# Optimization experiments

Hardware: AMD Instinct MI355X
Metric: run time of the kernel (lower is better)

## Reference

```python
import jax, jax.numpy as jnp
import numpy as np

HEADS = 8
EMBED = 64  # out_channels per head
N_OP = 100000
N_MC = 20000
N_EDGE = 300000
EPS = 1e-16  # matches PyG softmax denominator epsilon


def hetero_gat(x_src, x_dst, edge_index, W, att, n_dst):
    """GAT conv: gather -> per-edge score -> segment softmax over dst -> scatter-sum -> head mean.
    x_src: [Ns, F], x_dst: [Nd, F], edge_index: [2, E] (row0=src, row1=dst),
    W: [HEADS*EMBED, F], att: [1, HEADS, 2*EMBED].
    """
    hs = (x_src @ W.T).reshape(-1, HEADS, EMBED)  # [Ns,H,C]
    hd = (x_dst @ W.T).reshape(-1, HEADS, EMBED)  # [Nd,H,C]
    src, dst = edge_index[0], edge_index[1]
    x_j = hs[src]                                  # [E,H,C] (source/neighbor)
    x_i = hd[dst]                                  # [E,H,C] (destination)
    att_i = att[0, :, :EMBED]                      # [H,C] weights for x_i part of concat
    att_j = att[0, :, EMBED:]                      # [H,C] weights for x_j part
    # (cat([x_i,x_j],-1) * att).sum(-1) without materializing the concat
    alpha = jnp.einsum('ehc,hc->eh', x_i, att_i) + jnp.einsum('ehc,hc->eh', x_j, att_j)
    # segment softmax grouped by destination node
    m = jax.ops.segment_max(alpha, dst, num_segments=n_dst)  # [Nd,H]
    e = jnp.exp(alpha - m[dst])
    s = jax.ops.segment_sum(e, dst, num_segments=n_dst)      # [Nd,H]
    alpha = e / (s[dst] + EPS)                                # [E,H]
    msg = x_j * alpha[..., None]                              # [E,H,C]
    out = jax.ops.segment_sum(msg, dst, num_segments=n_dst)   # [Nd,H,C]
    return out.mean(axis=1)                                   # [Nd,C] multi-head mean


def setup_inputs() -> dict:
    key = jax.random.key(0)
    ks = jax.random.split(key, 12)
    op_nodes = jax.random.normal(ks[0], (N_OP, 4), dtype=jnp.float32)
    mc_nodes = jax.random.normal(ks[1], (N_MC, 2), dtype=jnp.float32)
    src = jax.random.randint(ks[2], (N_EDGE,), 0, N_OP)
    dst = jax.random.randint(ks[3], (N_EDGE,), 0, N_MC)
    edge_index_om = jnp.stack([src, dst]).astype(jnp.int64)
    g = 0.1
    params = {
        'W_op': jax.random.normal(ks[4], (EMBED, 4), dtype=jnp.float32) * g,
        'b_op': jnp.zeros((EMBED,), dtype=jnp.float32),
        'W_mc': jax.random.normal(ks[5], (EMBED, 2), dtype=jnp.float32) * g,
        'b_mc': jnp.zeros((EMBED,), dtype=jnp.float32),
        'W_om': jax.random.normal(ks[6], (HEADS * EMBED, EMBED), dtype=jnp.float32) * g,
        'att_om': jax.random.normal(ks[7], (1, HEADS, 2 * EMBED), dtype=jnp.float32) * g,
        'W_mo': jax.random.normal(ks[8], (HEADS * EMBED, EMBED), dtype=jnp.float32) * g,
        'att_mo': jax.random.normal(ks[9], (1, HEADS, 2 * EMBED), dtype=jnp.float32) * g,
    }
    return {'op_nodes': op_nodes, 'mc_nodes': mc_nodes, 'edge_index_om': edge_index_om, **params}


def reference(op_nodes, mc_nodes, edge_index_om, W_op, b_op, W_mc, b_mc,
              W_om, att_om, W_mo, att_mo):
    h_op = jax.nn.elu(op_nodes @ W_op.T + b_op)   # [N_OP, 64]
    h_mc = jax.nn.elu(mc_nodes @ W_mc.T + b_mc)   # [N_MC, 64]
    # op -> mc
    h_mc_new = hetero_gat(h_op, h_mc, edge_index_om, W_om, att_om, N_MC)
    h_mc = jax.nn.elu(h_mc + h_mc_new)
    # mc -> op (reversed edges)
    edge_index_mo = jnp.stack([edge_index_om[1], edge_index_om[0]])
    h_op_new = hetero_gat(h_mc, h_op, edge_index_mo, W_mo, att_mo, N_OP)
    h_op = jax.nn.elu(h_op + h_op_new)
    return (h_op, h_mc)
```

## Files before the change

kernel.cpp:

```cpp
#include <hip/hip_runtime.h>
#include <hip/hip_bf16.h>

using bf16 = __hip_bfloat16;
typedef __attribute__((ext_vector_type(8))) short short8;
typedef __attribute__((ext_vector_type(4))) float f32x4;

__device__ __forceinline__ unsigned short f2bf(float f) {
  bf16 h = __float2bfloat16(f);
  return *reinterpret_cast<unsigned short*>(&h);
}
__device__ __forceinline__ float bf2f(unsigned short u) {
  return __uint_as_float(((unsigned)u) << 16);
}

__device__ __forceinline__ float loadf(const void* p, int i, int is_f32) {
  if (is_f32) return ((const float*)p)[i];
  return __bfloat162float(((const bf16*)p)[i]);
}

__global__ __launch_bounds__(256) void init_kernel(
    const int* __restrict__ ei, const unsigned short* __restrict__ x,
    int* __restrict__ flags, int* __restrict__ cnt1, int n1,
    int* __restrict__ cnt2, int n2) {
  int t = threadIdx.x;
  int g = blockIdx.x * 256 + t;
  int stride = gridDim.x * 256;
  for (int i = g; i < n1; i += stride) cnt1[i] = 0;
  for (int i = g; i < n2; i += stride) cnt2[i] = 0;
  if (blockIdx.x == 0) {
    __shared__ int red[256];
    int o = 0, big = 0;
    for (int i = t; i < 2048; i += 256) {
      o |= ei[2 * i + 1];
      float v = __uint_as_float(((unsigned)x[2 * i]) << 16);
      if (!(fabsf(v) < 1000.f)) big = 1;
    }
    red[t] = o;
    __syncthreads();
    for (int d = 128; d > 0; d >>= 1) {
      if (t < d) red[t] |= red[t + d];
      __syncthreads();
    }
    int o_all = red[0];
    __syncthreads();
    red[t] = big;
    __syncthreads();
    for (int d = 128; d > 0; d >>= 1) {
      if (t < d) red[t] |= red[t + d];
      __syncthreads();
    }
    if (t == 0) {
      flags[0] = red[0];
      flags[1] = (o_all == 0) ? 1 : 0;
    }
  }
}

__device__ __forceinline__ int edge_src(const int* ei, int E, int e, int i64) {
  return i64 ? ei[2 * e] : ei[e];
}
__device__ __forceinline__ int edge_dst(const int* ei, int E, int e, int i64) {
  return i64 ? ei[2 * E + 2 * e] : ei[E + e];
}

template <int FIN>
__device__ __forceinline__ void node_body4(
    const void* x, const void* W, const void* b, int is_f32,
    const float* vj, bf16* h_out, float* ea_out, int n0, int N) {
  int lane = threadIdx.x & 63;
  float wreg[FIN];
#pragma unroll
  for (int f = 0; f < FIN; ++f) wreg[f] = loadf(W, lane * FIN + f, is_f32);
  float bias = loadf(b, lane, is_f32);
  float vjreg[8];
  if (ea_out) {
#pragma unroll
    for (int h = 0; h < 8; ++h) vjreg[h] = vj[h * 64 + lane];
  }
#pragma unroll
  for (int j = 0; j < 4; ++j) {
    int n = n0 + j;
    if (n >= N) break;
    float acc = bias;
#pragma unroll
    for (int f = 0; f < FIN; ++f)
      acc += loadf(x, n * FIN + f, is_f32) * wreg[f];
    float hv = acc > 0.f ? acc : expm1f(acc);
    h_out[(unsigned)(n << 6) + lane] = __float2bfloat16(hv);
    if (ea_out) {
      float p[8];
#pragma unroll
      for (int h = 0; h < 8; ++h) p[h] = hv * vjreg[h];
#pragma unroll
      for (int i = 0; i < 4; ++i) {
        float send = (lane & 4) ? p[i] : p[i + 4];
        float keep = (lane & 4) ? p[i + 4] : p[i];
        p[i] = keep + __shfl_xor(send, 4, 64);
      }
#pragma unroll
      for (int i = 0; i < 2; ++i) {
        float send = (lane & 2) ? p[i] : p[i + 2];
        float keep = (lane & 2) ? p[i + 2] : p[i];
        p[i] = keep + __shfl_xor(send, 2, 64);
      }
      {
        float send = (lane & 1) ? p[0] : p[1];
        float keep = (lane & 1) ? p[1] : p[0];
        p[0] = keep + __shfl_xor(send, 1, 64);
      }
      p[0] += __shfl_xor(p[0], 8, 64);
      p[0] += __shfl_xor(p[0], 16, 64);
      p[0] += __shfl_xor(p[0], 32, 64);
      if (lane < 8) ea_out[(unsigned)(n << 3) + lane] = __expf(p[0]);
    }
  }
}

__global__ __launch_bounds__(256) void front_kernel(
    const void* __restrict__ x_op, const void* __restrict__ W_op,
    const void* __restrict__ b_op, const void* __restrict__ x_mc,
    const void* __restrict__ W_mc, const void* __restrict__ b_mc,
    const void* __restrict__ W1, const void* __restrict__ att1,
    const void* __restrict__ W2, const void* __restrict__ att2,
    const int* __restrict__ ei, const int* __restrict__ flags,
    float* __restrict__ vj1, bf16* __restrict__ Wrt1, float* __restrict__ vj2,
    bf16* __restrict__ Wrt2, bf16* __restrict__ h_op,
    float* __restrict__ ea_op, bf16* __restrict__ h_mc,
    int* __restrict__ cnt_dst, int* __restrict__ cnt_src, int n_op, int n_mc,
    int E, int nbo, int nbm) {
  int bid = blockIdx.x;
  int is_f32 = flags[0];
  if (bid < nbo) {
    int n0 = bid * 16 + (threadIdx.x >> 6) * 4;
    if (n0 < n_op)
      node_body4<4>(x_op, W_op, b_op, is_f32, vj1, h_op, ea_op, n0, n_op);
  } else if (bid < nbo + nbm) {
    int n0 = (bid - nbo) * 16 + (threadIdx.x >> 6) * 4;
    if (n0 < n_mc)
      node_body4<2>(x_mc, W_mc, b_mc, is_f32, nullptr, h_mc, nullptr, n0, n_mc);
  } else if (bid < nbo + nbm + 256) {
    int pb = bid - nbo - nbm;
    int side = pb >= 128;
    const void* W = side ? W2 : W1;
    const void* att = side ? att2 : att1;
    float* vj = side ? vj2 : vj1;
    bf16* Wrt = side ? Wrt2 : Wrt1;
    int tt = (pb & 127) * 256 + threadIdx.x;
    if (tt < 32768) {
      int c = tt >> 9, k = tt & 511;
      int f = k >> 3, h = k & 7;
      Wrt[tt] = __float2bfloat16(loadf(W, ((h << 6) + c) * 64 + f, is_f32));
    }
    if (tt < 512) {
      int hh = tt >> 6, ff = tt & 63;
      float s = 0.f;
      for (int cc = 0; cc < 64; ++cc)
        s += loadf(att, hh * 128 + 64 + cc, is_f32) *
             loadf(W, ((hh << 6) + cc) * 64 + ff, is_f32);
      vj[tt] = s;
    }
  } else {
    int i64 = flags[1];
    int e = (bid - nbo - nbm - 256) * 256 + threadIdx.x;
    if (e < E) {
      atomicAdd(&cnt_dst[edge_dst(ei, E, e, i64)], 1);
      atomicAdd(&cnt_src[edge_src(ei, E, e, i64)], 1);
    }
  }
}

__global__ __launch_bounds__(256) void scan_bsum2(
    const int* __restrict__ cnt1, int n1, int nb1, const int* __restrict__ cnt2,
    int n2, int* __restrict__ bsum1, int* __restrict__ bsum2) {
  __shared__ int red[256];
  int t = threadIdx.x;
  int side = (int)blockIdx.x >= nb1;
  const int* cnt = side ? cnt2 : cnt1;
  int n = side ? n2 : n1;
  int blk = side ? (blockIdx.x - nb1) : blockIdx.x;
  int base = blk * 2048 + t * 8;
  int s = 0;
#pragma unroll
  for (int i = 0; i < 8; ++i)
    if (base + i < n) s += cnt[base + i];
  red[t] = s;
  __syncthreads();
  for (int d = 128; d > 0; d >>= 1) {
    if (t < d) red[t] += red[t + d];
    __syncthreads();
  }
  if (t == 0) (side ? bsum2 : bsum1)[blk] = red[0];
}

__global__ __launch_bounds__(256) void scan_write2(
    const int* __restrict__ cnt1, int n1, int nb1,
    const int* __restrict__ bsum1, int* __restrict__ offs1,
    int* __restrict__ cur1, const int* __restrict__ cnt2, int n2, int nb2,
    const int* __restrict__ bsum2, int* __restrict__ offs2,
    int* __restrict__ cur2) {
  __shared__ int red[256];
  __shared__ int base_s;
  int t = threadIdx.x;
  int side = (int)blockIdx.x >= nb1;
  const int* cnt = side ? cnt2 : cnt1;
  const int* bsum = side ? bsum2 : bsum1;
  int* offs = side ? offs2 : offs1;
  int* cur = side ? cur2 : cur1;
  int n = side ? n2 : n1;
  int nb = side ? nb2 : nb1;
  int blk = side ? (blockIdx.x - nb1) : blockIdx.x;
  if (t == 0) {
    int b = 0;
    for (int i = 0; i < blk; ++i) b += bsum[i];
    base_s = b;
  }
  int base = blk * 2048 + t * 8;
  int c[8];
  int s = 0;
#pragma unroll
  for (int i = 0; i < 8; ++i) {
    c[i] = (base + i < n) ? cnt[base + i] : 0;
    s += c[i];
  }
  red[t] = s;
  __syncthreads();
  for (int d = 1; d < 256; d <<= 1) {
    int v = red[t];
    int add = (t >= d) ? red[t - d] : 0;
    __syncthreads();
    red[t] = v + add;
    __syncthreads();
  }
  int run = base_s + red[t] - s;
#pragma unroll
  for (int i = 0; i < 8; ++i) {
    if (base + i < n) {
      offs[base + i] = run;
      cur[base + i] = run;
      run += c[i];
    }
  }
  if (blk == nb - 1 && t == 255) offs[n] = base_s + red[255];
}

__global__ __launch_bounds__(256) void fill_edges(
    const int* __restrict__ ei, int E, const int* __restrict__ flags,
    int* __restrict__ cur1, int* __restrict__ srcs1, int* __restrict__ cur2,
    int* __restrict__ srcs2) {
  int i64 = flags[1];
  int e = blockIdx.x * blockDim.x + threadIdx.x;
  if (e < E) {
    int s = edge_src(ei, E, e, i64), d = edge_dst(ei, E, e, i64);
    int p = atomicAdd(&cur1[d], 1);
    srcs1[p] = s;
    int q = atomicAdd(&cur2[s], 1);
    srcs2[q] = d;
  }
}

template <bool WRITE_AJ, bool WRITE_BF>
__global__ __launch_bounds__(256) void gat_fused(
    int Nd, const int* __restrict__ offs, const int* __restrict__ srcs,
    const float* __restrict__ ea, const bf16* __restrict__ h_src,
    const bf16* __restrict__ Wrt, const bf16* __restrict__ h_res,
    float* __restrict__ out_f32, bf16* __restrict__ out_bf,
    const float* __restrict__ vj_next, float* __restrict__ ea_next) {
  __shared__ __align__(16) unsigned short Zl[16 * 520];
  __shared__ int srcs_sw[4][65];
  __shared__ __align__(16) float ew_s[4][528];
  float(*ajp)[16][8] = reinterpret_cast<float(*)[16][8]>(&ew_s[0][0]);

  int t = threadIdx.x;
  int wv = t >> 6, lane = t & 63;
  int d0 = blockIdx.x * 16;
  int sj = lane >> 4;
  int fq = lane & 15;

  int dlo = d0 + wv * 4;
  int wo0 = offs[min(dlo + 0, Nd)];
  int wo1 = offs[min(dlo + 1, Nd)];
  int wo2 = offs[min(dlo + 2, Nd)];
  int wo3 = offs[min(dlo + 3, Nd)];
  int wo4 = offs[min(dlo + 4, Nd)];
  int woj = sj == 0 ? wo0 : sj == 1 ? wo1 : sj == 2 ? wo2 : wo3;
  int woj1 = sj == 0 ? wo1 : sj == 1 ? wo2 : sj == 2 ? wo3 : wo4;

  float z[8][4];
#pragma unroll
  for (int h = 0; h < 8; ++h)
#pragma unroll
    for (int f = 0; f < 4; ++f) z[h][f] = 0.f;
  float s8[8];
#pragma unroll
  for (int h = 0; h < 8; ++h) s8[h] = 0.f;

  const unsigned short* hsrc_u = (const unsigned short*)h_src;

  for (int cb = wo0; cb < wo4; cb += 64) {
    int cn = min(64, wo4 - cb);
    for (int i = lane; i < cn + 1; i += 64)
      srcs_sw[wv][i] = (i < cn) ? srcs[cb + i] : 0;
    for (int i = lane; i < (cn + 1) * 8; i += 64) {
      int e = i >> 3;
      int src2 = (e < cn) ? srcs[cb + e] : 0;
      ew_s[wv][i] = (e < cn) ? ea[((unsigned)src2 << 3) + (i & 7)] : 0.f;
    }
    int c0 = max(cb, woj) - cb;
    int e1 = min(cb + cn, woj1) - cb;
    int rl = max(e1 - c0, 0);
    int rmax = max(rl, __shfl_xor(rl, 16, 64));
    rmax = max(rmax, __shfl_xor(rmax, 32, 64));
    for (int r0 = 0; r0 < rmax; r0 += 4) {
      int i2q[4];
      ushort4 uq[4];
#pragma unroll
      for (int q = 0; q < 4; ++q) {
        int r = r0 + q;
        int i2 = (r < rl) ? (c0 + r) : cn;
        i2q[q] = i2;
        int src = srcs_sw[wv][i2];
        uq[q] = *(const ushort4*)(hsrc_u + (((unsigned)src) << 6) + (fq << 2));
      }
#pragma unroll
      for (int q = 0; q < 4; ++q) {
        int i2 = i2q[q];
        float4 lo4 = *(const float4*)&ew_s[wv][i2 * 8];
        float4 hi4 = *(const float4*)&ew_s[wv][i2 * 8 + 4];
        float x0 = bf2f(uq[q].x), x1 = bf2f(uq[q].y);
        float x2 = bf2f(uq[q].z), x3 = bf2f(uq[q].w);
        z[0][0] += lo4.x * x0; z[0][1] += lo4.x * x1; z[0][2] += lo4.x * x2; z[0][3] += lo4.x * x3;
        z[1][0] += lo4.y * x0; z[1][1] += lo4.y * x1; z[1][2] += lo4.y * x2; z[1][3] += lo4.y * x3;
        z[2][0] += lo4.z * x0; z[2][1] += lo4.z * x1; z[2][2] += lo4.z * x2; z[2][3] += lo4.z * x3;
        z[3][0] += lo4.w * x0; z[3][1] += lo4.w * x1; z[3][2] += lo4.w * x2; z[3][3] += lo4.w * x3;
        z[4][0] += hi4.x * x0; z[4][1] += hi4.x * x1; z[4][2] += hi4.x * x2; z[4][3] += hi4.x * x3;
        z[5][0] += hi4.y * x0; z[5][1] += hi4.y * x1; z[5][2] += hi4.y * x2; z[5][3] += hi4.y * x3;
        z[6][0] += hi4.z * x0; z[6][1] += hi4.z * x1; z[6][2] += hi4.z * x2; z[6][3] += hi4.z * x3;
        z[7][0] += hi4.w * x0; z[7][1] += hi4.w * x1; z[7][2] += hi4.w * x2; z[7][3] += hi4.w * x3;
        s8[0] += lo4.x; s8[1] += lo4.y; s8[2] += lo4.z; s8[3] += lo4.w;
        s8[4] += hi4.x; s8[5] += hi4.y; s8[6] += hi4.z; s8[7] += hi4.w;
      }
    }
  }

  float si[8];
#pragma unroll
  for (int h = 0; h < 8; ++h) si[h] = s8[h] > 0.f ? 1.f / s8[h] : 0.f;
  int row = wv * 4 + sj;
#pragma unroll
  for (int fi = 0; fi < 4; ++fi) {
    int4 pk;
    pk.x = ((int)f2bf(z[1][fi] * si[1]) << 16) | f2bf(z[0][fi] * si[0]);
    pk.y = ((int)f2bf(z[3][fi] * si[3]) << 16) | f2bf(z[2][fi] * si[2]);
    pk.z = ((int)f2bf(z[5][fi] * si[5]) << 16) | f2bf(z[4][fi] * si[4]);
    pk.w = ((int)f2bf(z[7][fi] * si[7]) << 16) | f2bf(z[6][fi] * si[6]);
    *(int4*)&Zl[row * 520 + (fq * 4 + fi) * 8] = pk;
  }

  int arow = lane & 15;
  int kg = lane >> 4;
  int col = wv * 16 + arow;
  float res[4];
#pragma unroll
  for (int r = 0; r < 4; ++r) {
    int d = d0 + kg * 4 + r;
    res[r] = (d < Nd)
                 ? __bfloat162float(h_res[(unsigned)(d << 6) + col])
                 : 0.f;
  }
  __syncthreads();

  f32x4 acc = {0.f, 0.f, 0.f, 0.f};
#pragma unroll
  for (int kt = 0; kt < 16; ++kt) {
    int kbase = kt * 32 + kg * 8;
    short8 a = *(const short8*)&Zl[arow * 520 + kbase];
    short8 b = *(const short8*)&Wrt[(unsigned)((wv * 16 + arow) * 512 + kbase)];
    acc = __builtin_amdgcn_mfma_f32_16x16x32_bf16(a, b, acc, 0, 0, 0);
  }

  float o_r[4];
#pragma unroll
  for (int r = 0; r < 4; ++r) {
    int d = d0 + kg * 4 + r;
    float o = 0.f;
    if (d < Nd) {
      float v = res[r] + 0.125f * acc[r];
      o = v > 0.f ? v : expm1f(v);
      out_f32[(unsigned)(d << 6) + col] = o;
      if (WRITE_BF) out_bf[(unsigned)(d << 6) + col] = __float2bfloat16(o);
    }
    o_r[r] = o;
  }

  if (WRITE_AJ) {
#pragma unroll
    for (int r = 0; r < 4; ++r) {
      int dloc = kg * 4 + r;
      float p[8];
#pragma unroll
      for (int h = 0; h < 8; ++h) p[h] = o_r[r] * vj_next[h * 64 + col];
#pragma unroll
      for (int i = 0; i < 4; ++i) {
        float send = (arow & 4) ? p[i] : p[i + 4];
        float keep = (arow & 4) ? p[i + 4] : p[i];
        p[i] = keep + __shfl_xor(send, 4, 64);
      }
#pragma unroll
      for (int i = 0; i < 2; ++i) {
        float send = (arow & 2) ? p[i] : p[i + 2];
        float keep = (arow & 2) ? p[i + 2] : p[i];
        p[i] = keep + __shfl_xor(send, 2, 64);
      }
      {
        float send = (arow & 1) ? p[0] : p[1];
        float keep = (arow & 1) ? p[1] : p[0];
        p[0] = keep + __shfl_xor(send, 1, 64);
      }
      p[0] += __shfl_xor(p[0], 8, 64);
      if (arow < 8) ajp[wv][dloc][arow] = p[0];
    }
    __syncthreads();
    if (t < 128) {
      int dloc = t >> 3, h = t & 7;
      int d = d0 + dloc;
      if (d < Nd) {
        float s = ajp[0][dloc][h] + ajp[1][dloc][h] + ajp[2][dloc][h] +
                  ajp[3][dloc][h];
        ea_next[(unsigned)(d << 3) + h] = __expf(s);
      }
    }
  }
}

extern "C" void kernel_launch(void* const* d_in, const int* in_sizes, int n_in,
                              void* d_out, int out_size, void* d_ws,
                              size_t ws_size, hipStream_t stream) {
  const void* op_nodes = d_in[0];
  const void* mc_nodes = d_in[1];
  const int* ei        = (const int*)d_in[2];
  const void* W_op     = d_in[3];
  const void* b_op     = d_in[4];
  const void* W_mc     = d_in[5];
  const void* b_mc     = d_in[6];
  const void* W_om     = d_in[7];
  const void* att_om   = d_in[8];
  const void* W_mo     = d_in[9];
  const void* att_mo   = d_in[10];

  int n_op = in_sizes[0] / 4;
  int n_mc = in_sizes[1] / 2;
  int E    = in_sizes[2] / 2;

  char* ws = (char*)d_ws;
  size_t off = 0;
  auto alloc = [&](size_t bytes) -> void* {
    void* p = ws + off;
    off = (off + bytes + 255) & ~(size_t)255;
    return p;
  };
  int* flags   = (int*)alloc(16);
  bf16* h_op   = (bf16*)alloc((size_t)n_op * 64 * 2);
  bf16* h_mc   = (bf16*)alloc((size_t)n_mc * 64 * 2);
  bf16* h_mc2  = (bf16*)alloc((size_t)n_mc * 64 * 2);
  float* ea_op = (float*)alloc((size_t)n_op * 8 * 4);
  float* ea_mc = (float*)alloc((size_t)n_mc * 8 * 4);
  float* vj_om = (float*)alloc(512 * 4);
  float* vj_mo = (float*)alloc(512 * 4);
  bf16* Wrt_om = (bf16*)alloc(32768 * 2);
  bf16* Wrt_mo = (bf16*)alloc(32768 * 2);
  int* cnt1  = (int*)alloc((size_t)n_mc * 4);
  int* cnt2  = (int*)alloc((size_t)n_op * 4);
  int* offs1 = (int*)alloc((size_t)(n_mc + 1) * 4);
  int* cur1  = (int*)alloc((size_t)n_mc * 4);
  int* srcs1 = (int*)alloc((size_t)E * 4);
  int* offs2 = (int*)alloc((size_t)(n_op + 1) * 4);
  int* cur2  = (int*)alloc((size_t)n_op * 4);
  int* srcs2 = (int*)alloc((size_t)E * 4);
  int* bsum1 = (int*)alloc(256 * 4);
  int* bsum2 = (int*)alloc(256 * 4);

  float* out_op = (float*)d_out;
  float* out_mc = out_op + (size_t)n_op * 64;

  init_kernel<<<512, 256, 0, stream>>>(ei, (const unsigned short*)op_nodes,
                                       flags, cnt1, n_mc, cnt2, n_op);

  int nbo = (n_op + 15) / 16, nbm = (n_mc + 15) / 16;
  int nbe = (E + 255) / 256;
  front_kernel<<<nbo + nbm + 256 + nbe, 256, 0, stream>>>(
      op_nodes, W_op, b_op, mc_nodes, W_mc, b_mc, W_om, att_om, W_mo, att_mo,
      ei, flags, vj_om, Wrt_om, vj_mo, Wrt_mo, h_op, ea_op, h_mc, cnt1, cnt2,
      n_op, n_mc, E, nbo, nbm);

  int nb1 = (n_mc + 2047) / 2048, nb2 = (n_op + 2047) / 2048;
  scan_bsum2<<<nb1 + nb2, 256, 0, stream>>>(cnt1, n_mc, nb1, cnt2, n_op, bsum1,
                                            bsum2);
  scan_write2<<<nb1 + nb2, 256, 0, stream>>>(cnt1, n_mc, nb1, bsum1, offs1,
                                             cur1, cnt2, n_op, nb2, bsum2,
                                             offs2, cur2);
  fill_edges<<<nbe, 256, 0, stream>>>(ei, E, flags, cur1, srcs1, cur2, srcs2);

  gat_fused<true, true><<<(n_mc + 15) / 16, 256, 0, stream>>>(
      n_mc, offs1, srcs1, ea_op, h_op, Wrt_om, h_mc, out_mc, h_mc2, vj_mo,
      ea_mc);
  gat_fused<false, false><<<(n_op + 15) / 16, 256, 0, stream>>>(
      n_op, offs2, srcs2, ea_mc, h_mc2, Wrt_mo, h_op, out_op, (bf16*)nullptr,
      (const float*)nullptr, (float*)nullptr);
}
```

Measured before the change: 233.5 us.

## Store edge attention weights in bf16 and gather them directly per edge

Per-source exp attention weights (ea) are now stored as bf16 instead of fp32, halving their footprint. The gather loop no longer stages source indices and weights into per-wave shared memory in 64-edge chunks. Each lane now reads its own source indices and 16-byte weight vectors straight from global memory. This removes the shared staging, its redundant cooperative loads, and the shared-memory footprint, at the cost of more scattered global reads of srcs and ea per lane and reduced precision in the softmax weights.

```diff
diff --git a/kernel.cpp b/kernel.cpp
--- a/kernel.cpp
+++ b/kernel.cpp
@@ -66,7 +66,7 @@
 template <int FIN>
 __device__ __forceinline__ void node_body4(
     const void* x, const void* W, const void* b, int is_f32,
-    const float* vj, bf16* h_out, float* ea_out, int n0, int N) {
+    const float* vj, bf16* h_out, unsigned short* ea_out, int n0, int N) {
   int lane = threadIdx.x & 63;
   float wreg[FIN];
 #pragma unroll
@@ -111,7 +111,7 @@
       p[0] += __shfl_xor(p[0], 8, 64);
       p[0] += __shfl_xor(p[0], 16, 64);
       p[0] += __shfl_xor(p[0], 32, 64);
-      if (lane < 8) ea_out[(unsigned)(n << 3) + lane] = __expf(p[0]);
+      if (lane < 8) ea_out[(unsigned)(n << 3) + lane] = f2bf(__expf(p[0]));
     }
   }
 }
@@ -125,7 +125,7 @@
     const int* __restrict__ ei, const int* __restrict__ flags,
     float* __restrict__ vj1, bf16* __restrict__ Wrt1, float* __restrict__ vj2,
     bf16* __restrict__ Wrt2, bf16* __restrict__ h_op,
-    float* __restrict__ ea_op, bf16* __restrict__ h_mc,
+    unsigned short* __restrict__ ea_op, bf16* __restrict__ h_mc,
     int* __restrict__ cnt_dst, int* __restrict__ cnt_src, int n_op, int n_mc,
     int E, int nbo, int nbm) {
   int bid = blockIdx.x;
@@ -261,14 +261,12 @@
 template <bool WRITE_AJ, bool WRITE_BF>
 __global__ __launch_bounds__(256) void gat_fused(
     int Nd, const int* __restrict__ offs, const int* __restrict__ srcs,
-    const float* __restrict__ ea, const bf16* __restrict__ h_src,
+    const unsigned short* __restrict__ ea, const bf16* __restrict__ h_src,
     const bf16* __restrict__ Wrt, const bf16* __restrict__ h_res,
     float* __restrict__ out_f32, bf16* __restrict__ out_bf,
-    const float* __restrict__ vj_next, float* __restrict__ ea_next) {
+    const float* __restrict__ vj_next, unsigned short* __restrict__ ea_next) {
   __shared__ __align__(16) unsigned short Zl[16 * 520];
-  __shared__ int srcs_sw[4][65];
-  __shared__ __align__(16) float ew_s[4][528];
-  float(*ajp)[16][8] = reinterpret_cast<float(*)[16][8]>(&ew_s[0][0]);
+  __shared__ float ajp[4][16][8];
 
   int t = threadIdx.x;
   int wv = t >> 6, lane = t & 63;
@@ -284,6 +282,7 @@
   int wo4 = offs[min(dlo + 4, Nd)];
   int woj = sj == 0 ? wo0 : sj == 1 ? wo1 : sj == 2 ? wo2 : wo3;
   int woj1 = sj == 0 ? wo1 : sj == 1 ? wo2 : sj == 2 ? wo3 : wo4;
+  int nj = woj1 - woj;
 
   float z[8][4];
 #pragma unroll
@@ -296,48 +295,40 @@
 
   const unsigned short* hsrc_u = (const unsigned short*)h_src;
 
-  for (int cb = wo0; cb < wo4; cb += 64) {
-    int cn = min(64, wo4 - cb);
-    for (int i = lane; i < cn + 1; i += 64)
-      srcs_sw[wv][i] = (i < cn) ? srcs[cb + i] : 0;
-    for (int i = lane; i < (cn + 1) * 8; i += 64) {
-      int e = i >> 3;
-      int src2 = (e < cn) ? srcs[cb + e] : 0;
-      ew_s[wv][i] = (e < cn) ? ea[((unsigned)src2 << 3) + (i & 7)] : 0.f;
-    }
-    int c0 = max(cb, woj) - cb;
-    int e1 = min(cb + cn, woj1) - cb;
-    int rl = max(e1 - c0, 0);
-    int rmax = max(rl, __shfl_xor(rl, 16, 64));
-    rmax = max(rmax, __shfl_xor(rmax, 32, 64));
-    for (int r0 = 0; r0 < rmax; r0 += 4) {
-      int i2q[4];
-      ushort4 uq[4];
-#pragma unroll
-      for (int q = 0; q < 4; ++q) {
-        int r = r0 + q;
-        int i2 = (r < rl) ? (c0 + r) : cn;
-        i2q[q] = i2;
-        int src = srcs_sw[wv][i2];
-        uq[q] = *(const ushort4*)(hsrc_u + (((unsigned)src) << 6) + (fq << 2));
-      }
-#pragma unroll
-      for (int q = 0; q < 4; ++q) {
-        int i2 = i2q[q];
-        float4 lo4 = *(const float4*)&ew_s[wv][i2 * 8];
-        float4 hi4 = *(const float4*)&ew_s[wv][i2 * 8 + 4];
-        float x0 = bf2f(uq[q].x), x1 = bf2f(uq[q].y);
-        float x2 = bf2f(uq[q].z), x3 = bf2f(uq[q].w);
-        z[0][0] += lo4.x * x0; z[0][1] += lo4.x * x1; z[0][2] += lo4.x * x2; z[0][3] += lo4.x * x3;
-        z[1][0] += lo4.y * x0; z[1][1] += lo4.y * x1; z[1][2] += lo4.y * x2; z[1][3] += lo4.y * x3;
-        z[2][0] += lo4.z * x0; z[2][1] += lo4.z * x1; z[2][2] += lo4.z * x2; z[2][3] += lo4.z * x3;
-        z[3][0] += lo4.w * x0; z[3][1] += lo4.w * x1; z[3][2] += lo4.w * x2; z[3][3] += lo4.w * x3;
-        z[4][0] += hi4.x * x0; z[4][1] += hi4.x * x1; z[4][2] += hi4.x * x2; z[4][3] += hi4.x * x3;
-        z[5][0] += hi4.y * x0; z[5][1] += hi4.y * x1; z[5][2] += hi4.y * x2; z[5][3] += hi4.y * x3;
-        z[6][0] += hi4.z * x0; z[6][1] += hi4.z * x1; z[6][2] += hi4.z * x2; z[6][3] += hi4.z * x3;
-        z[7][0] += hi4.w * x0; z[7][1] += hi4.w * x1; z[7][2] += hi4.w * x2; z[7][3] += hi4.w * x3;
-        s8[0] += lo4.x; s8[1] += lo4.y; s8[2] += lo4.z; s8[3] += lo4.w;
-        s8[4] += hi4.x; s8[5] += hi4.y; s8[6] += hi4.z; s8[7] += hi4.w;
+  int rmax = max(nj, __shfl_xor(nj, 16, 64));
+  rmax = max(rmax, __shfl_xor(rmax, 32, 64));
+
+  for (int r0 = 0; r0 < rmax; r0 += 4) {
+    unsigned srcq[4];
+#pragma unroll
+    for (int q = 0; q < 4; ++q) {
+      int r = r0 + q;
+      srcq[q] = (r < nj) ? (unsigned)srcs[woj + r] : 0u;
+    }
+    ushort4 uq[4];
+    short8 eq[4];
+#pragma unroll
+    for (int q = 0; q < 4; ++q) {
+      unsigned s = srcq[q];
+      uq[q] = *(const ushort4*)(hsrc_u + (s << 6) + (fq << 2));
+      eq[q] = *(const short8*)(ea + (s << 3));
+    }
+#pragma unroll
+    for (int q = 0; q < 4; ++q) {
+      bool act = (r0 + q) < nj;
+      float w[8];
+#pragma unroll
+      for (int h = 0; h < 8; ++h)
+        w[h] = act ? bf2f((unsigned short)eq[q][h]) : 0.f;
+      float x0 = bf2f(uq[q].x), x1 = bf2f(uq[q].y);
+      float x2 = bf2f(uq[q].z), x3 = bf2f(uq[q].w);
+#pragma unroll
+      for (int h = 0; h < 8; ++h) {
+        z[h][0] += w[h] * x0;
+        z[h][1] += w[h] * x1;
+        z[h][2] += w[h] * x2;
+        z[h][3] += w[h] * x3;
+        s8[h] += w[h];
       }
     }
   }
@@ -363,9 +354,8 @@
 #pragma unroll
   for (int r = 0; r < 4; ++r) {
     int d = d0 + kg * 4 + r;
-    res[r] = (d < Nd)
-                 ? __bfloat162float(h_res[(unsigned)(d << 6) + col])
-                 : 0.f;
+    res[r] =
+        (d < Nd) ? __bfloat162float(h_res[(unsigned)(d << 6) + col]) : 0.f;
   }
   __syncthreads();
 
@@ -426,7 +416,7 @@
       if (d < Nd) {
         float s = ajp[0][dloc][h] + ajp[1][dloc][h] + ajp[2][dloc][h] +
                   ajp[3][dloc][h];
-        ea_next[(unsigned)(d << 3) + h] = __expf(s);
+        ea_next[(unsigned)(d << 3) + h] = f2bf(__expf(s));
       }
     }
   }
@@ -462,8 +452,8 @@
   bf16* h_op   = (bf16*)alloc((size_t)n_op * 64 * 2);
   bf16* h_mc   = (bf16*)alloc((size_t)n_mc * 64 * 2);
   bf16* h_mc2  = (bf16*)alloc((size_t)n_mc * 64 * 2);
-  float* ea_op = (float*)alloc((size_t)n_op * 8 * 4);
-  float* ea_mc = (float*)alloc((size_t)n_mc * 8 * 4);
+  unsigned short* ea_op = (unsigned short*)alloc((size_t)n_op * 8 * 2);
+  unsigned short* ea_mc = (unsigned short*)alloc((size_t)n_mc * 8 * 2);
   float* vj_om = (float*)alloc(512 * 4);
   float* vj_mo = (float*)alloc(512 * 4);
   bf16* Wrt_om = (bf16*)alloc(32768 * 2);
@@ -505,5 +495,5 @@
       ea_mc);
   gat_fused<false, false><<<(n_op + 15) / 16, 256, 0, stream>>>(
       n_op, offs2, srcs2, ea_mc, h_mc2, Wrt_mo, h_op, out_op, (bf16*)nullptr,
-      (const float*)nullptr, (float*)nullptr);
-}
+      (const float*)nullptr, (unsigned short*)nullptr);
+}
```

Result: faster. 207.6 us, median of 3 (-11.1%).
